# Performance work log

Hardware: AMD Instinct MI355X
Metric: run time of the kernel (lower is better)

The kernel has to match this reference:

```python
import jax, jax.numpy as jnp
import numpy as np
import math

NUM_HEADS = 8
DROPOUT_RATE = 0.1
D_IN = 32
D_PROJ = 32 * 16  # 512
B, SQ, SK = 8, 2048, 2048


def setup_inputs() -> dict:
    key = jax.random.key(0)
    ks = jax.random.split(key, 10)
    inv = 1.0 / math.sqrt(D_IN)
    return {
        "query": jax.random.normal(ks[0], (B, SQ, D_IN), dtype=jnp.float32),
        "key": jax.random.normal(ks[1], (B, SK, D_IN), dtype=jnp.float32),
        "value": jax.random.normal(ks[2], (B, SK, D_IN), dtype=jnp.float32),
        "mask": jax.random.randint(ks[3], (B, 1, 1, SK), 0, 2, dtype=jnp.int32),
        "Wq": jax.random.normal(ks[4], (D_PROJ, D_IN), dtype=jnp.float32) * inv,
        "bq": jax.random.normal(ks[5], (D_PROJ,), dtype=jnp.float32) * 0.02,
        "Wk": jax.random.normal(ks[6], (D_PROJ, D_IN), dtype=jnp.float32) * inv,
        "bk": jax.random.normal(ks[7], (D_PROJ,), dtype=jnp.float32) * 0.02,
        "Wv": jax.random.normal(ks[8], (D_PROJ, D_IN), dtype=jnp.float32) * inv,
        "bv": jax.random.normal(ks[9], (D_PROJ,), dtype=jnp.float32) * 0.02,
    }


def _split_heads(x):
    # [B, S, H*D] -> [B, H, S, D]
    b, s, _ = x.shape
    return x.reshape(b, s, NUM_HEADS, D_PROJ // NUM_HEADS).transpose(0, 2, 1, 3)


def reference(query, key, value, mask, Wq, bq, Wk, bk, Wv, bv):
    q = _split_heads(query @ Wq.T + bq)   # [B, H, Sq, D]
    k = _split_heads(key @ Wk.T + bk)     # [B, H, Sk, D]
    v = _split_heads(value @ Wv.T + bv)   # [B, H, Sk, D]

    head_dim = q.shape[-1]
    # mask only feeds this scalar; max(1-p, (1-p)/(Sm2*Sm3)) == 1-p for Sm2*Sm3 >= 1
    keep = 1.0 - DROPOUT_RATE
    scale_factor = jnp.maximum(jnp.float32(keep),
                               jnp.float32(keep / (mask.shape[2] * mask.shape[3])))

    scores = jnp.einsum("bhqd,bhkd->bhqk", q, k) * (scale_factor / math.sqrt(head_dim))
    probs = jax.nn.softmax(scores, axis=-1)
    # dropout treated as identity (eval mode) for a deterministic reference
    out = jnp.einsum("bhqk,bhkd->bhqd", probs, v)  # [B, H, Sq, D]
    b, h, sq, d = out.shape
    return out.transpose(0, 2, 1, 3).reshape(b, sq, h * d)
```

## Files before the change

### kernel.cpp

```cpp
#include <hip/hip_runtime.h>
#include <hip/hip_bf16.h>
#include <math.h>

#define B_   8
#define H_   8
#define S_   2048
#define D_   64
#define BH_  64
#define DPROJ_ 512

typedef __attribute__((ext_vector_type(8)))  _Float16 f16x8;
typedef __attribute__((ext_vector_type(4)))  float    f32x4;
typedef __attribute__((ext_vector_type(16))) float    f32x16;
typedef __attribute__((ext_vector_type(4)))  int      i32x4;

static __device__ __forceinline__ short f16bits(float f) {
    return __builtin_bit_cast(short, (_Float16)f);
}

static __device__ __forceinline__ f16x8 load8_f32_f16(const float* p) {
    const float4 a = ((const float4*)p)[0];
    const float4 b = ((const float4*)p)[1];
    f16x8 r;
    r[0] = (_Float16)a.x; r[1] = (_Float16)a.y; r[2] = (_Float16)a.z; r[3] = (_Float16)a.w;
    r[4] = (_Float16)b.x; r[5] = (_Float16)b.y; r[6] = (_Float16)b.z; r[7] = (_Float16)b.w;
    return r;
}

#if __has_builtin(__builtin_amdgcn_exp2f)
#define EXP2(x) __builtin_amdgcn_exp2f(x)
#else
#define EXP2(x) exp2f(x)
#endif

static __device__ __forceinline__ void pl32swap(unsigned int& a, unsigned int& b) {
#if __has_builtin(__builtin_amdgcn_permlane32_swap)
    auto r = __builtin_amdgcn_permlane32_swap((int)a, (int)b, false, false);
    a = (unsigned int)r[0];
    b = (unsigned int)r[1];
#else
    const bool lh0 = ((threadIdx.x & 63) < 32);
    unsigned int xa = (unsigned int)__shfl_xor((int)a, 32);
    unsigned int xb = (unsigned int)__shfl_xor((int)b, 32);
    unsigned int na = lh0 ? a : xb;
    unsigned int nb = lh0 ? xa : b;
    a = na; b = nb;
#endif
}

#define QKST 520

__global__ __launch_bounds__(256)
void proj_kernel(const float* __restrict__ query, const float* __restrict__ key,
                 const float* __restrict__ value,
                 const float* __restrict__ Wq, const float* __restrict__ bq,
                 const float* __restrict__ Wk, const float* __restrict__ bk,
                 const float* __restrict__ Wv, const float* __restrict__ bv,
                 short* __restrict__ qws, short* __restrict__ kws,
                 short* __restrict__ vws)
{
    __shared__ __align__(16) short shbuf[16384];

    const int tid  = threadIdx.x;
    const int wave = tid >> 6;
    const int lane = tid & 63;
    const int n    = lane & 15;
    const int quad = lane >> 4;
    const int kind = blockIdx.y;

    if (kind < 2) {
        short* tile = shbuf;
        const int r0   = blockIdx.x * 16;
        const int b    = r0 >> 11;
        const int s0   = r0 & 2047;
        const float QS = 0.16230319188537014f;

        const float* X    = kind ? key : query;
        const float* W    = kind ? Wk  : Wq;
        const float* bias = kind ? bk  : bq;
        short*       ows  = kind ? kws : qws;

        f16x8 af = load8_f32_f16(X + (r0 + n) * 32 + quad * 8);
        #pragma unroll
        for (int i = 0; i < 8; ++i) {
            const int c0 = wave * 128 + i * 16;
            f16x8 bfr = load8_f32_f16(W + (c0 + n) * 32 + quad * 8);
            f32x4 acc = {0.f, 0.f, 0.f, 0.f};
            acc = __builtin_amdgcn_mfma_f32_16x16x32_f16(af, bfr, acc, 0, 0, 0);
            const int c = c0 + n;
            const float bsf = bias[c];
            #pragma unroll
            for (int r = 0; r < 4; ++r) {
                float v = acc[r] + bsf;
                if (kind == 0) v *= QS;
                tile[(quad * 4 + r) * QKST + c] = f16bits(v);
            }
        }
        __syncthreads();

        #pragma unroll
        for (int k = 0; k < 4; ++k) {
            const int slot = k * 256 + tid;
            const int li   = slot & 7;
            const int chunk= slot >> 3;
            const int row  = chunk & 15;
            const int hd   = chunk >> 4;
            uint4 vv = *(const uint4*)(tile + row * QKST + hd * 64 + li * 8);
            const int bh = b * 8 + hd;
            if (kind == 0) {
                *(uint4*)(ows + ((size_t)bh * S_ + s0 + row) * 64 + li * 8) = vv;
            } else {
                const int s = s0 + row;
                *(uint4*)(ows + (size_t)bh * (S_ * 64)
                              + (size_t)(s >> 5) * 2048 + li * 256 + (s & 31) * 8) = vv;
            }
        }
    } else {
        if (blockIdx.x >= 256) return;
        short* vtile = shbuf;
        const int r0   = blockIdx.x * 64;
        const int b    = r0 >> 11;
        const int s0   = r0 & 2047;
        const int sub  = wave >> 1;
        const int sh   = (wave & 1) * 16;

        #pragma unroll
        for (int half = 0; half < 2; ++half) {
            const int cbh = half * 256;
            f16x8 bfr = load8_f32_f16(value + (r0 + sub * 32 + sh + n) * 32 + quad * 8);
            #pragma unroll
            for (int i = 0; i < 16; ++i) {
                const int c0 = cbh + i * 16;
                f16x8 af = load8_f32_f16(Wv + (c0 + n) * 32 + quad * 8);
                f32x4 acc = {0.f, 0.f, 0.f, 0.f};
                acc = __builtin_amdgcn_mfma_f32_16x16x32_f16(af, bfr, acc, 0, 0, 0);
                #pragma unroll
                for (int r = 0; r < 4; ++r) {
                    const int dc = c0 + quad * 4 + r;
                    float v = acc[r] + bv[dc];
                    vtile[(sub * 256 + (dc - cbh)) * 32 + sh + n] = f16bits(v);
                }
            }
            __syncthreads();

            #pragma unroll
            for (int k = 0; k < 8; ++k) {
                const int slot = k * 256 + tid;
                const int li   = slot & 3;
                const int cl   = (slot >> 2) & 255;
                const int sb   = slot >> 10;
                const int c    = cbh + cl;
                const int bh   = b * 8 + (c >> 6);
                const int d    = c & 63;
                const int stile= (s0 >> 5) + sb;
                uint4 vv = *(const uint4*)(vtile + (sb * 256 + cl) * 32 + li * 8);
                *(uint4*)(vws + (size_t)bh * (S_ * 64)
                              + (size_t)stile * 2048
                              + ((d >> 5) * 4 + (li >> 1) * 2 + (li & 1)) * 256
                              + (d & 31) * 8) = vv;
            }
            if (half == 0) __syncthreads();
        }
    }
}

#define OTS 36

static __device__ __forceinline__ void flash_compute(
    const f16x8 (&kf)[4], const f16x8 (&va)[4],
    const f16x8 (&qb)[2][4], const f32x16& z16,
    f32x16 (&o)[2][2], float (&pl)[2])
{
    #pragma unroll
    for (int qg = 0; qg < 2; ++qg) {
        f32x16 st = __builtin_amdgcn_mfma_f32_32x32x16_f16(kf[0], qb[qg][0], z16, 0, 0, 0);
        #pragma unroll
        for (int h = 1; h < 4; ++h)
            st = __builtin_amdgcn_mfma_f32_32x32x16_f16(kf[h], qb[qg][h], st, 0, 0, 0);

        float p[16];
        #pragma unroll
        for (int r = 0; r < 16; ++r) p[r] = EXP2(st[r]);
        float s01 = (p[0]+p[1]) + (p[2]+p[3]);
        float s23 = (p[4]+p[5]) + (p[6]+p[7]);
        float s45 = (p[8]+p[9]) + (p[10]+p[11]);
        float s67 = (p[12]+p[13]) + (p[14]+p[15]);
        pl[qg] += (s01 + s23) + (s45 + s67);

        unsigned int pk[8];
        #pragma unroll
        for (int i = 0; i < 8; ++i)
            pk[i] = __builtin_bit_cast(unsigned int,
                      __builtin_amdgcn_cvt_pkrtz(p[2 * i], p[2 * i + 1]));
        pl32swap(pk[0], pk[2]);
        pl32swap(pk[1], pk[3]);
        pl32swap(pk[4], pk[6]);
        pl32swap(pk[5], pk[7]);

        i32x4 bi0, bi1;
        bi0[0] = (int)pk[0]; bi0[1] = (int)pk[1];
        bi0[2] = (int)pk[2]; bi0[3] = (int)pk[3];
        bi1[0] = (int)pk[4]; bi1[1] = (int)pk[5];
        bi1[2] = (int)pk[6]; bi1[3] = (int)pk[7];
        f16x8 bf0 = __builtin_bit_cast(f16x8, bi0);
        f16x8 bf1 = __builtin_bit_cast(f16x8, bi1);

        #pragma unroll
        for (int t = 0; t < 2; ++t) {
            o[qg][t] = __builtin_amdgcn_mfma_f32_32x32x16_f16(va[t * 2 + 0], bf0, o[qg][t], 0, 0, 0);
            o[qg][t] = __builtin_amdgcn_mfma_f32_32x32x16_f16(va[t * 2 + 1], bf1, o[qg][t], 0, 0, 0);
        }
    }
}

__global__ __launch_bounds__(256, 2)
void flash_kernel(const short* __restrict__ qws, const short* __restrict__ kws,
                  const short* __restrict__ vws, float* __restrict__ out)
{
    __shared__ __align__(16) float olds[4 * 32 * OTS];

    const int tid  = threadIdx.x;
    const int wave = tid >> 6;
    const int lane = tid & 63;
    const int m32  = lane & 31;
    const int lh   = lane >> 5;
    const int koff = lh * 8;
    const int bh   = blockIdx.x;
    const int q0   = blockIdx.y * 256 + wave * 64;

    const short* qbase = qws + (size_t)bh * S_ * D_;
    const short* kfb   = kws + (size_t)bh * (S_ * 64);
    const short* vfb   = vws + (size_t)bh * (S_ * 64);
    const int loff = lh * 256 + m32 * 8;

    f16x8 qb[2][4];
    #pragma unroll
    for (int qg = 0; qg < 2; ++qg)
        #pragma unroll
        for (int h = 0; h < 4; ++h)
            qb[qg][h] = *(const f16x8*)(qbase + (q0 + qg * 32 + m32) * D_ + h * 16 + koff);

    f32x16 z16;
    #pragma unroll
    for (int r = 0; r < 16; ++r) z16[r] = 0.f;

    f32x16 o[2][2];
    float  pl[2] = {0.f, 0.f};
    #pragma unroll
    for (int qg = 0; qg < 2; ++qg)
        #pragma unroll
        for (int t = 0; t < 2; ++t)
            o[qg][t] = z16;

    #define LOADFRAGS(T, kf, va) do {                                        \
        const short* kp_ = kfb + (size_t)(T) * 2048 + loff;                  \
        const short* vp_ = vfb + (size_t)(T) * 2048 + loff;                  \
        kf[0] = *(const f16x8*)(kp_);                                        \
        kf[1] = *(const f16x8*)(kp_ + 512);                                  \
        kf[2] = *(const f16x8*)(kp_ + 1024);                                 \
        kf[3] = *(const f16x8*)(kp_ + 1536);                                 \
        va[0] = *(const f16x8*)(vp_);                                        \
        va[1] = *(const f16x8*)(vp_ + 512);                                  \
        va[2] = *(const f16x8*)(vp_ + 1024);                                 \
        va[3] = *(const f16x8*)(vp_ + 1536);                                 \
    } while (0)

    f16x8 kfA[4], vaA[4], kfB[4], vaB[4];
    LOADFRAGS(0, kfA, vaA);

    for (int it = 0; it < 64; it += 2) {
        LOADFRAGS(it + 1, kfB, vaB);
        flash_compute(kfA, vaA, qb, z16, o, pl);
        if (it + 2 < 64)
            LOADFRAGS(it + 2, kfA, vaA);
        flash_compute(kfB, vaB, qb, z16, o, pl);
    }
    #undef LOADFRAGS

    const int b = bh >> 3, h = bh & 7;
    float* ow = olds + wave * (32 * OTS);
    #pragma unroll
    for (int qg = 0; qg < 2; ++qg) {
        float rs = pl[qg] + __shfl_xor(pl[qg], 32);
        float rl = 1.0f / rs;
        #pragma unroll
        for (int t = 0; t < 2; ++t) {
            const f32x16& ot = o[qg][t];
            #pragma unroll
            for (int g = 0; g < 4; ++g) {
                f32x4 w;
                w[0] = ot[g * 4 + 0] * rl;
                w[1] = ot[g * 4 + 1] * rl;
                w[2] = ot[g * 4 + 2] * rl;
                w[3] = ot[g * 4 + 3] * rl;
                *(f32x4*)(ow + m32 * OTS + 8 * g + 4 * lh) = w;
            }
            #pragma unroll
            for (int c = 0; c < 4; ++c) {
                const int row = (lane >> 3) + 8 * c;
                f32x4 v = *(const f32x4*)(ow + row * OTS + (lane & 7) * 4);
                const int sq = q0 + qg * 32 + row;
                *(f32x4*)(out + ((size_t)(b * S_ + sq)) * DPROJ_
                              + h * 64 + t * 32 + (lane & 7) * 4) = v;
            }
        }
    }
}

extern "C" void kernel_launch(void* const* d_in, const int* in_sizes, int n_in,
                              void* d_out, int out_size, void* d_ws, size_t ws_size,
                              hipStream_t stream)
{
    const float* query = (const float*)d_in[0];
    const float* key   = (const float*)d_in[1];
    const float* value = (const float*)d_in[2];
    const float* Wq = (const float*)d_in[4];
    const float* bq = (const float*)d_in[5];
    const float* Wk = (const float*)d_in[6];
    const float* bk = (const float*)d_in[7];
    const float* Wv = (const float*)d_in[8];
    const float* bv = (const float*)d_in[9];

    float* out = (float*)d_out;
    short* ws  = (short*)d_ws;
    const size_t TSZ = (size_t)BH_ * S_ * D_;
    short* qws = ws;
    short* kws = ws + TSZ;
    short* vws = ws + 2 * TSZ;

    proj_kernel<<<dim3((B_ * S_) / 16, 3), 256, 0, stream>>>(
        query, key, value, Wq, bq, Wk, bk, Wv, bv, qws, kws, vws);
    flash_kernel<<<dim3(BH_, S_ / 256), 256, 0, stream>>>(qws, kws, vws, out);
}
```

Before: 184.8 us.

## Software-pipeline QK MFMA of next tile with softmax/PV of current tile

Splits the per-tile flash step into a QK-score phase and an exp/sum/PV phase. The loop is reordered so the QK MFMAs for tile t+1 are issued before the exponentials and PV MFMAs of tile t, with K and V fragment loads interleaved between phases. This aims to hide the exp and convert work behind independent MFMA work and give the loads more latency slack. In exchange it keeps two score accumulators live, which raises register pressure and could reduce occupancy.

```diff
diff --git a/kernel.cpp b/kernel.cpp
--- a/kernel.cpp
+++ b/kernel.cpp
@@ -166,32 +166,38 @@
 
 #define OTS 36
 
-static __device__ __forceinline__ void flash_compute(
-    const f16x8 (&kf)[4], const f16x8 (&va)[4],
-    const f16x8 (&qb)[2][4], const f32x16& z16,
+static __device__ __forceinline__ void qk_phase(
+    const f16x8 (&kf)[4], const f16x8 (&qb)[2][4], const f32x16& z16,
+    f32x16 (&st)[2])
+{
+    #pragma unroll
+    for (int qg = 0; qg < 2; ++qg) {
+        st[qg] = __builtin_amdgcn_mfma_f32_32x32x16_f16(kf[0], qb[qg][0], z16, 0, 0, 0);
+        #pragma unroll
+        for (int h = 1; h < 4; ++h)
+            st[qg] = __builtin_amdgcn_mfma_f32_32x32x16_f16(kf[h], qb[qg][h], st[qg], 0, 0, 0);
+    }
+}
+
+static __device__ __forceinline__ void finish_phase(
+    f32x16 (&st)[2], const f16x8 (&va)[4],
     f32x16 (&o)[2][2], float (&pl)[2])
 {
     #pragma unroll
     for (int qg = 0; qg < 2; ++qg) {
-        f32x16 st = __builtin_amdgcn_mfma_f32_32x32x16_f16(kf[0], qb[qg][0], z16, 0, 0, 0);
-        #pragma unroll
-        for (int h = 1; h < 4; ++h)
-            st = __builtin_amdgcn_mfma_f32_32x32x16_f16(kf[h], qb[qg][h], st, 0, 0, 0);
-
-        float p[16];
-        #pragma unroll
-        for (int r = 0; r < 16; ++r) p[r] = EXP2(st[r]);
-        float s01 = (p[0]+p[1]) + (p[2]+p[3]);
-        float s23 = (p[4]+p[5]) + (p[6]+p[7]);
-        float s45 = (p[8]+p[9]) + (p[10]+p[11]);
-        float s67 = (p[12]+p[13]) + (p[14]+p[15]);
+        #pragma unroll
+        for (int r = 0; r < 16; ++r) st[qg][r] = EXP2(st[qg][r]);
+        float s01 = (st[qg][0]+st[qg][1]) + (st[qg][2]+st[qg][3]);
+        float s23 = (st[qg][4]+st[qg][5]) + (st[qg][6]+st[qg][7]);
+        float s45 = (st[qg][8]+st[qg][9]) + (st[qg][10]+st[qg][11]);
+        float s67 = (st[qg][12]+st[qg][13]) + (st[qg][14]+st[qg][15]);
         pl[qg] += (s01 + s23) + (s45 + s67);
 
         unsigned int pk[8];
         #pragma unroll
         for (int i = 0; i < 8; ++i)
             pk[i] = __builtin_bit_cast(unsigned int,
-                      __builtin_amdgcn_cvt_pkrtz(p[2 * i], p[2 * i + 1]));
+                      __builtin_amdgcn_cvt_pkrtz(st[qg][2 * i], st[qg][2 * i + 1]));
         pl32swap(pk[0], pk[2]);
         pl32swap(pk[1], pk[3]);
         pl32swap(pk[4], pk[6]);
@@ -252,13 +258,15 @@
         for (int t = 0; t < 2; ++t)
             o[qg][t] = z16;
 
-    #define LOADFRAGS(T, kf, va) do {                                        \
+    #define LOADK(T, kf) do {                                                \
         const short* kp_ = kfb + (size_t)(T) * 2048 + loff;                  \
-        const short* vp_ = vfb + (size_t)(T) * 2048 + loff;                  \
         kf[0] = *(const f16x8*)(kp_);                                        \
         kf[1] = *(const f16x8*)(kp_ + 512);                                  \
         kf[2] = *(const f16x8*)(kp_ + 1024);                                 \
         kf[3] = *(const f16x8*)(kp_ + 1536);                                 \
+    } while (0)
+    #define LOADV(T, va) do {                                                \
+        const short* vp_ = vfb + (size_t)(T) * 2048 + loff;                  \
         va[0] = *(const f16x8*)(vp_);                                        \
         va[1] = *(const f16x8*)(vp_ + 512);                                  \
         va[2] = *(const f16x8*)(vp_ + 1024);                                 \
@@ -266,16 +274,29 @@
     } while (0)
 
     f16x8 kfA[4], vaA[4], kfB[4], vaB[4];
-    LOADFRAGS(0, kfA, vaA);
-
-    for (int it = 0; it < 64; it += 2) {
-        LOADFRAGS(it + 1, kfB, vaB);
-        flash_compute(kfA, vaA, qb, z16, o, pl);
-        if (it + 2 < 64)
-            LOADFRAGS(it + 2, kfA, vaA);
-        flash_compute(kfB, vaB, qb, z16, o, pl);
-    }
-    #undef LOADFRAGS
+    f32x16 stA[2], stB[2];
+
+    LOADK(0, kfA);  LOADV(0, vaA);
+    LOADK(1, kfB);  LOADV(1, vaB);
+    qk_phase(kfA, qb, z16, stA);
+
+    for (int it = 0; it < 62; it += 2) {
+        qk_phase(kfB, qb, z16, stB);
+        LOADK(it + 2, kfA);
+        finish_phase(stA, vaA, o, pl);
+        LOADV(it + 2, vaA);
+
+        qk_phase(kfA, qb, z16, stA);
+        LOADK(it + 3, kfB);
+        finish_phase(stB, vaB, o, pl);
+        LOADV(it + 3, vaB);
+    }
+    qk_phase(kfB, qb, z16, stB);
+    finish_phase(stA, vaA, o, pl);
+    finish_phase(stB, vaB, o, pl);
+
+    #undef LOADK
+    #undef LOADV
 
     const int b = bh >> 3, h = bh & 7;
     float* ow = olds + wave * (32 * OTS);
```

Measured after the change: 191.3 us. 3.5% more time.
